# Performance work log

Measured on AMD Instinct MI355X. Metric: run time of the kernel, lower is better.

Reference implementation:

```python
import jax, jax.numpy as jnp
import numpy as np

T, H, W_, CIN, LAT, HID, OUT, NHL = 32, 64, 64, 3, 256, 256, 3, 3
OMEGA = 30.0  # SIREN sine frequency


def _uniform(key, shape, fan_in):
    b = np.sqrt(6.0 / fan_in) / OMEGA
    return jax.random.uniform(key, shape, jnp.float32, -b, b)


def setup_inputs() -> dict:
    key = jax.random.key(0)
    ks = jax.random.split(key, 10)
    return {
        "coords": jax.random.normal(ks[0], (T, H, W_, CIN), jnp.float32),
        "latents": jax.random.normal(ks[1], (T, LAT), jnp.float32),
        # shared SIREN weights (nf_net): W stored as (out, in) like nn.Linear
        "W0": _uniform(ks[2], (HID, CIN), CIN),
        "b0": jnp.zeros((HID,), jnp.float32),
        "Wh": _uniform(ks[3], (NHL, HID, HID), HID),
        "bh": jnp.zeros((NHL, HID), jnp.float32),
        "Wf": _uniform(ks[4], (OUT, HID), HID),
        "bf": jnp.zeros((OUT,), jnp.float32),
        # hypernet weight generators (hw_net), no bias
        "HW0": _uniform(ks[5], (HID * CIN, LAT), LAT),
        "HWh": _uniform(ks[6], (NHL, HID * HID, LAT), LAT),
        # hypernet bias generators (hb_net), no bias
        "HB": _uniform(ks[7], (NHL + 1, HID, LAT), LAT),
    }


def reference(coords, latents, W0, b0, Wh, bh, Wf, bf, HW0, HWh, HB):
    t = latents.shape[0]
    # per-frame hyper biases for all layers: (t, NHL+1, HID)
    hb = jnp.einsum('tl,khl->tkh', latents, HB)
    # layer 0: per-frame weight (t, HID, CIN)
    hw0 = (latents @ HW0.T).reshape(t, HID, CIN)
    x = coords  # (t,h,w,CIN)
    x = (x @ W0.T + b0
         + jnp.einsum('thwi,toi->thwo', x, hw0)
         + hb[:, 0][:, None, None, :])
    x = jnp.sin(OMEGA * x)
    for i in range(NHL):
        hw = (latents @ HWh[i].T).reshape(t, HID, HID)  # (t, HID, HID)
        x = (x @ Wh[i].T + bh[i]
             + jnp.einsum('thwi,toi->thwo', x, hw)
             + hb[:, i + 1][:, None, None, :])
        x = jnp.sin(OMEGA * x)
    return x @ Wf.T + bf  # (t,h,w,OUT)
```

## Files before the change

### kernel.cpp

```cpp
#include <hip/hip_runtime.h>
#include <cstdint>
#include <cstddef>

typedef __attribute__((ext_vector_type(8))) _Float16 f16x8;
typedef __attribute__((ext_vector_type(16))) float f32x16;

#define LO_SCALE 2048.0f
#define LO_INV   (1.0f / 2048.0f)

union H8 { f16x8 v; _Float16 h[8]; };

__global__ __launch_bounds__(256) void kab(
    const float* __restrict__ latents, const float* __restrict__ W0,
    const float* __restrict__ b0, const float* __restrict__ bh,
    const float* __restrict__ HW0, const float* __restrict__ HB,
    const float* __restrict__ Wh, const float* __restrict__ HWh,
    _Float16* __restrict__ w0blob, float* __restrict__ beff,
    _Float16* __restrict__ whblob) {
  __shared__ float lat_t[8192];
  int tid = threadIdx.x, bid = blockIdx.x;

  if (bid >= 768) {
    int id = (bid - 768) * 256 + tid;
    if (id < 32768) {
      int t = id >> 10, rem = id & 1023;
      int r2 = rem & 127, part = r2 >> 6, lane = r2 & 63;
      int nf = rem >> 7;
      int o = nf * 32 + (lane & 31), kc = lane >> 5;
      const float* lat = latents + t * 256;
      H8 outv;
#pragma unroll
      for (int j = 0; j < 8; ++j) outv.h[j] = (_Float16)0.0f;
#pragma unroll
      for (int j = 0; j < 8; ++j) {
        int i = kc * 8 + j;
        if (i < 3) {
          const float* row = HW0 + (o * 3 + i) * 256;
          float s = W0[o * 3 + i];
          for (int k = 0; k < 256; k += 4)
            s += row[k] * lat[k] + row[k + 1] * lat[k + 1] +
                 row[k + 2] * lat[k + 2] + row[k + 3] * lat[k + 3];
          _Float16 hi = (_Float16)s;
          outv.h[j] = part ? (_Float16)((s - (float)hi) * LO_SCALE) : hi;
        }
      }
      *(f16x8*)(w0blob + (size_t)id * 8) = outv.v;
    } else {
      int v = id - 32768;
      int t = v >> 10, k = (v >> 8) & 3, hm = v & 255;
      float base = (k == 0) ? b0[hm] : bh[(k - 1) * 256 + hm];
      const float* lat = latents + t * 256;
      const float* row = HB + (size_t)(k * 256 + hm) * 256;
      float s = base;
      for (int kk = 0; kk < 256; kk += 4)
        s += row[kk] * lat[kk] + row[kk + 1] * lat[kk + 1] +
             row[kk + 2] * lat[kk + 2] + row[kk + 3] * lat[kk + 3];
      beff[v] = s;
    }
    return;
  }

  int h = bid & 1, ks = (bid >> 1) & 15, nf = (bid >> 5) & 7, l = bid >> 8;

  {
    int f = tid >> 3, kb = (tid & 7) * 32;
#pragma unroll
    for (int m = 0; m < 32; m += 4) {
      float4 v = *(const float4*)(latents + f * 256 + kb + m);
      lat_t[(kb + m + 0) * 32 + f] = v.x;
      lat_t[(kb + m + 1) * 32 + f] = v.y;
      lat_t[(kb + m + 2) * 32 + f] = v.z;
      lat_t[(kb + m + 3) * 32 + f] = v.w;
    }
  }
  __syncthreads();

  int oo = tid >> 3, jj = tid & 7;
  int o = nf * 32 + oo;
  int i = ks * 16 + h * 8 + jj;
  int r = o * 256 + i;
  const float* rowp = HWh + ((size_t)l * 65536 + (size_t)r) * 256;

  float acc[32];
#pragma unroll
  for (int f = 0; f < 32; ++f) acc[f] = 0.f;

  float curf[16], nxtf[16];
#pragma unroll
  for (int q = 0; q < 4; ++q)
    *(float4*)(curf + q * 4) = *(const float4*)(rowp + q * 4);

  for (int kc = 0; kc < 16; ++kc) {
    if (kc < 15) {
#pragma unroll
      for (int q = 0; q < 4; ++q)
        *(float4*)(nxtf + q * 4) = *(const float4*)(rowp + (kc + 1) * 16 + q * 4);
    }
    const float* lp = lat_t + kc * 512;
#pragma unroll
    for (int m = 0; m < 16; ++m) {
      float hw = curf[m];
#pragma unroll
      for (int fq = 0; fq < 8; ++fq) {
        float4 lv = *(const float4*)(lp + m * 32 + fq * 4);
        acc[fq * 4 + 0] += hw * lv.x;
        acc[fq * 4 + 1] += hw * lv.y;
        acc[fq * 4 + 2] += hw * lv.z;
        acc[fq * 4 + 3] += hw * lv.w;
      }
    }
#pragma unroll
    for (int q = 0; q < 16; ++q) curf[q] = nxtf[q];
  }

  float whv = Wh[l * 65536 + r];
  size_t cbase = (size_t)(nf * 16 + ks) * 1024 + (size_t)h * 256 + (size_t)tid;
#pragma unroll
  for (int t = 0; t < 32; ++t) {
    float w = acc[t] + whv;
    _Float16 hi = (_Float16)w;
    _Float16 lo = (_Float16)((w - (float)hi) * LO_SCALE);
    size_t b = (size_t)(t * 3 + l) * 131072 + cbase;
    whblob[b] = hi;
    whblob[b + 512] = lo;
  }
}

__global__ __launch_bounds__(256, 2) void kb_siren(
    const float* __restrict__ coords, const _Float16* __restrict__ whblob,
    const _Float16* __restrict__ w0blob, const float* __restrict__ beff,
    const float* __restrict__ Wf, const float* __restrict__ bf,
    float* __restrict__ out) {
  __shared__ _Float16 xs_hi[64 * 264];
  __shared__ _Float16 xs_lo[64 * 264];
  __shared__ float wf_s[768];
  __shared__ float red[768];
  int tid = threadIdx.x;
  int bid0 = blockIdx.x;
  int bid = (bid0 & 7) * 256 + (bid0 >> 3);
  int t = bid >> 6, tile = bid & 63;
  int wv = tid >> 6, lane = tid & 63, col = lane & 31, h = lane >> 5;

  if (tid < 192) *(float4*)(wf_s + tid * 4) = *(const float4*)(Wf + tid * 4);
  if (tid < 64) {
    const float* cp = coords + (size_t)(t * 4096 + tile * 64 + tid) * 3;
    float c0 = cp[0], c1 = cp[1], c2 = cp[2];
    H8 hv, lv, z;
#pragma unroll
    for (int j = 0; j < 8; ++j) { hv.h[j] = (_Float16)0.f; lv.h[j] = (_Float16)0.f; z.h[j] = (_Float16)0.f; }
    _Float16 h0 = (_Float16)c0, h1 = (_Float16)c1, h2 = (_Float16)c2;
    hv.h[0] = h0; hv.h[1] = h1; hv.h[2] = h2;
    lv.h[0] = (_Float16)((c0 - (float)h0) * LO_SCALE);
    lv.h[1] = (_Float16)((c1 - (float)h1) * LO_SCALE);
    lv.h[2] = (_Float16)((c2 - (float)h2) * LO_SCALE);
    *(f16x8*)(xs_hi + tid * 264) = hv.v;
    *(f16x8*)(xs_lo + tid * 264) = lv.v;
    *(f16x8*)(xs_hi + tid * 264 + 8) = z.v;
    *(f16x8*)(xs_lo + tid * 264 + 8) = z.v;
  }
  __syncthreads();

  f32x16 accA[2][2], accB[2][2];

  auto init_bias = [&](int bk) {
#pragma unroll
    for (int fr = 0; fr < 2; ++fr) {
      const float* bp = beff + ((t * 4 + bk) << 8) + (wv * 2 + fr) * 32 + h * 4;
#pragma unroll
      for (int rq = 0; rq < 4; ++rq) {
        float4 bvv = *(const float4*)(bp + rq * 8);
        float ba[4];
        *(float4*)ba = bvv;
#pragma unroll
        for (int q = 0; q < 4; ++q) {
          accA[fr][0][rq * 4 + q] = ba[q];
          accA[fr][1][rq * 4 + q] = ba[q];
          accB[fr][0][rq * 4 + q] = 0.f;
          accB[fr][1][rq * 4 + q] = 0.f;
        }
      }
    }
  };

  auto aload4 = [&](const _Float16* blobL, int NS, int ks,
                    f16x8& a0h, f16x8& a0l, f16x8& a1h, f16x8& a1l) {
    const _Float16* p0 = blobL + (size_t)(((wv * 2 + 0) * NS + ks) * 2) * 512 + lane * 8;
    const _Float16* p1 = blobL + (size_t)(((wv * 2 + 1) * NS + ks) * 2) * 512 + lane * 8;
    a0h = *(const f16x8*)p0;
    a0l = *(const f16x8*)(p0 + 512);
    a1h = *(const f16x8*)p1;
    a1l = *(const f16x8*)(p1 + 512);
  };

  auto mfma_step = [&](f16x8 a0h, f16x8 a0l, f16x8 a1h, f16x8 a1l, int ks) {
#pragma unroll
    for (int pf = 0; pf < 2; ++pf) {
      int off = (pf * 32 + col) * 264 + ks * 16 + h * 8;
      f16x8 bh_ = *(const f16x8*)(xs_hi + off);
      f16x8 bl_ = *(const f16x8*)(xs_lo + off);
      accA[0][pf] = __builtin_amdgcn_mfma_f32_32x32x16_f16(a0h, bh_, accA[0][pf], 0, 0, 0);
      accB[0][pf] = __builtin_amdgcn_mfma_f32_32x32x16_f16(a0h, bl_, accB[0][pf], 0, 0, 0);
      accB[0][pf] = __builtin_amdgcn_mfma_f32_32x32x16_f16(a0l, bh_, accB[0][pf], 0, 0, 0);
      accA[1][pf] = __builtin_amdgcn_mfma_f32_32x32x16_f16(a1h, bh_, accA[1][pf], 0, 0, 0);
      accB[1][pf] = __builtin_amdgcn_mfma_f32_32x32x16_f16(a1h, bl_, accB[1][pf], 0, 0, 0);
      accB[1][pf] = __builtin_amdgcn_mfma_f32_32x32x16_f16(a1l, bh_, accB[1][pf], 0, 0, 0);
    }
  };

  auto epilogue = [&]() {
#pragma unroll
    for (int fr = 0; fr < 2; ++fr)
#pragma unroll
      for (int pf = 0; pf < 2; ++pf)
#pragma unroll
        for (int r = 0; r < 16; ++r)
          accA[fr][pf][r] = __sinf(fmaf(accB[fr][pf][r], 30.0f * LO_INV, 30.0f * accA[fr][pf][r]));
    __syncthreads();
#pragma unroll
    for (int fr = 0; fr < 2; ++fr)
#pragma unroll
      for (int pf = 0; pf < 2; ++pf)
#pragma unroll
        for (int g = 0; g < 2; ++g) {
          float seq[8];
#pragma unroll
          for (int q = 0; q < 4; ++q) {
            float oa = accA[fr][pf][8 * g + q];
            float ob = accA[fr][pf][8 * g + 4 + q];
            float send = h ? oa : ob;
            float recv = __shfl_xor(send, 32, 64);
            seq[q]     = h ? recv : oa;
            seq[4 + q] = h ? ob : recv;
          }
          H8 hv, lv;
#pragma unroll
          for (int j = 0; j < 8; ++j) {
            _Float16 hi = (_Float16)seq[j];
            hv.h[j] = hi;
            lv.h[j] = (_Float16)((seq[j] - (float)hi) * LO_SCALE);
          }
          int off = (pf * 32 + col) * 264 + wv * 64 + fr * 32 + g * 16 + h * 8;
          *(f16x8*)(xs_hi + off) = hv.v;
          *(f16x8*)(xs_lo + off) = lv.v;
        }
    __syncthreads();
  };

  const _Float16* bl0 = whblob + (size_t)(t * 3) * 131072;
  f16x8 c0h, c0l, c1h, c1l, n0h, n0l, n1h, n1l;

  init_bias(0);
  aload4(w0blob + (size_t)t * 8192, 1, 0, c0h, c0l, c1h, c1l);
  mfma_step(c0h, c0l, c1h, c1l, 0);
  aload4(bl0, 16, 0, c0h, c0l, c1h, c1l);
  epilogue();

#pragma unroll
  for (int li = 0; li < 3; ++li) {
    init_bias(li + 1);
    const _Float16* bl = whblob + (size_t)(t * 3 + li) * 131072;
    const _Float16* bln = whblob + (size_t)(t * 3 + li + 1) * 131072;
#pragma unroll
    for (int ks2 = 0; ks2 < 8; ++ks2) {
      int ksA = ks2 * 2, ksB = ks2 * 2 + 1;
      aload4(bl, 16, ksB, n0h, n0l, n1h, n1l);
      mfma_step(c0h, c0l, c1h, c1l, ksA);
      if (ksB < 15) {
        aload4(bl, 16, ksB + 1, c0h, c0l, c1h, c1l);
      } else if (li < 2) {
        aload4(bln, 16, 0, c0h, c0l, c1h, c1l);
      }
      mfma_step(n0h, n0l, n1h, n1l, ksB);
    }
    epilogue();
  }

  {
    float pc0 = 0.f, pc1 = 0.f, pc2 = 0.f;
    int px = tid & 63, kq = tid >> 6;
#pragma unroll
    for (int cc = 0; cc < 8; ++cc) {
      int k0 = kq * 64 + cc * 8;
      H8 hv, lv;
      hv.v = *(const f16x8*)(xs_hi + px * 264 + k0);
      lv.v = *(const f16x8*)(xs_lo + px * 264 + k0);
#pragma unroll
      for (int j = 0; j < 8; ++j) {
        float xv = (float)hv.h[j] + (float)lv.h[j] * LO_INV;
        pc0 += xv * wf_s[k0 + j];
        pc1 += xv * wf_s[256 + k0 + j];
        pc2 += xv * wf_s[512 + k0 + j];
      }
    }
    red[kq * 192 + px * 3 + 0] = pc0;
    red[kq * 192 + px * 3 + 1] = pc1;
    red[kq * 192 + px * 3 + 2] = pc2;
    __syncthreads();
    if (tid < 192) {
      int p2 = tid / 3, c = tid - p2 * 3;
      float s = bf[c];
#pragma unroll
      for (int q = 0; q < 4; ++q) s += red[q * 192 + p2 * 3 + c];
      out[(size_t)(t * 4096 + tile * 64 + p2) * 3 + c] = s;
    }
  }
}

extern "C" void kernel_launch(void* const* d_in, const int* in_sizes, int n_in,
                              void* d_out, int out_size, void* d_ws, size_t ws_size,
                              hipStream_t stream) {
  const float* coords  = (const float*)d_in[0];
  const float* latents = (const float*)d_in[1];
  const float* W0      = (const float*)d_in[2];
  const float* b0      = (const float*)d_in[3];
  const float* Wh      = (const float*)d_in[4];
  const float* bh      = (const float*)d_in[5];
  const float* Wf      = (const float*)d_in[6];
  const float* bf      = (const float*)d_in[7];
  const float* HW0     = (const float*)d_in[8];
  const float* HWh     = (const float*)d_in[9];
  const float* HB      = (const float*)d_in[10];
  float* outp = (float*)d_out;

  char* w = (char*)d_ws;
  _Float16* whblob = (_Float16*)w;
  _Float16* w0blob = (_Float16*)(w + 25165824);
  float*    beff   = (float*)(w + 25690112);

  kab<<<1024, 256, 0, stream>>>(latents, W0, b0, bh, HW0, HB, Wh, HWh,
                                w0blob, beff, whblob);
  kb_siren<<<2048, 256, 0, stream>>>(coords, whblob, w0blob, beff, Wf, bf, outp);
}
```

Measured before the change: 230.0 us.

## Prescale weights by omega/2pi, use fract+v_sin, drop shuffles in epilogue stores

```diff
diff --git a/kernel.cpp b/kernel.cpp
--- a/kernel.cpp
+++ b/kernel.cpp
@@ -3,12 +3,15 @@
 #include <cstddef>
 
 typedef __attribute__((ext_vector_type(8))) _Float16 f16x8;
+typedef __attribute__((ext_vector_type(2))) __fp16 h2;
 typedef __attribute__((ext_vector_type(16))) float f32x16;
 
 #define LO_SCALE 2048.0f
 #define LO_INV   (1.0f / 2048.0f)
+#define OMEGA_SC 4.774648292756860f
 
 union H8 { f16x8 v; _Float16 h[8]; };
+union U2 { h2 v[2]; uint2 u; };
 
 __global__ __launch_bounds__(256) void kab(
     const float* __restrict__ latents, const float* __restrict__ W0,
@@ -40,6 +43,7 @@
           for (int k = 0; k < 256; k += 4)
             s += row[k] * lat[k] + row[k + 1] * lat[k + 1] +
                  row[k + 2] * lat[k + 2] + row[k + 3] * lat[k + 3];
+          s *= OMEGA_SC;
           _Float16 hi = (_Float16)s;
           outv.h[j] = part ? (_Float16)((s - (float)hi) * LO_SCALE) : hi;
         }
@@ -55,7 +59,7 @@
       for (int kk = 0; kk < 256; kk += 4)
         s += row[kk] * lat[kk] + row[kk + 1] * lat[kk + 1] +
              row[kk + 2] * lat[kk + 2] + row[kk + 3] * lat[kk + 3];
-      beff[v] = s;
+      beff[v] = s * OMEGA_SC;
     }
     return;
   }
@@ -117,7 +121,7 @@
   size_t cbase = (size_t)(nf * 16 + ks) * 1024 + (size_t)h * 256 + (size_t)tid;
 #pragma unroll
   for (int t = 0; t < 32; ++t) {
-    float w = acc[t] + whv;
+    float w = (acc[t] + whv) * OMEGA_SC;
     _Float16 hi = (_Float16)w;
     _Float16 lo = (_Float16)((w - (float)hi) * LO_SCALE);
     size_t b = (size_t)(t * 3 + l) * 131072 + cbase;
@@ -148,11 +152,11 @@
     H8 hv, lv, z;
 #pragma unroll
     for (int j = 0; j < 8; ++j) { hv.h[j] = (_Float16)0.f; lv.h[j] = (_Float16)0.f; z.h[j] = (_Float16)0.f; }
-    _Float16 h0 = (_Float16)c0, h1 = (_Float16)c1, h2 = (_Float16)c2;
-    hv.h[0] = h0; hv.h[1] = h1; hv.h[2] = h2;
+    _Float16 h0 = (_Float16)c0, h1 = (_Float16)c1, h2_ = (_Float16)c2;
+    hv.h[0] = h0; hv.h[1] = h1; hv.h[2] = h2_;
     lv.h[0] = (_Float16)((c0 - (float)h0) * LO_SCALE);
     lv.h[1] = (_Float16)((c1 - (float)h1) * LO_SCALE);
-    lv.h[2] = (_Float16)((c2 - (float)h2) * LO_SCALE);
+    lv.h[2] = (_Float16)((c2 - (float)h2_) * LO_SCALE);
     *(f16x8*)(xs_hi + tid * 264) = hv.v;
     *(f16x8*)(xs_lo + tid * 264) = lv.v;
     *(f16x8*)(xs_hi + tid * 264 + 8) = z.v;
@@ -207,6 +211,13 @@
     }
   };
 
+  auto sin2pi = [](float x) {
+    float f, r;
+    asm("v_fract_f32 %0, %1" : "=v"(f) : "v"(x));
+    asm("v_sin_f32 %0, %1" : "=v"(r) : "v"(f));
+    return r;
+  };
+
   auto epilogue = [&]() {
 #pragma unroll
     for (int fr = 0; fr < 2; ++fr)
@@ -214,35 +225,35 @@
       for (int pf = 0; pf < 2; ++pf)
 #pragma unroll
         for (int r = 0; r < 16; ++r)
-          accA[fr][pf][r] = __sinf(fmaf(accB[fr][pf][r], 30.0f * LO_INV, 30.0f * accA[fr][pf][r]));
+          accA[fr][pf][r] = sin2pi(fmaf(accB[fr][pf][r], LO_INV, accA[fr][pf][r]));
     __syncthreads();
 #pragma unroll
     for (int fr = 0; fr < 2; ++fr)
 #pragma unroll
-      for (int pf = 0; pf < 2; ++pf)
-#pragma unroll
-        for (int g = 0; g < 2; ++g) {
-          float seq[8];
-#pragma unroll
-          for (int q = 0; q < 4; ++q) {
-            float oa = accA[fr][pf][8 * g + q];
-            float ob = accA[fr][pf][8 * g + 4 + q];
-            float send = h ? oa : ob;
-            float recv = __shfl_xor(send, 32, 64);
-            seq[q]     = h ? recv : oa;
-            seq[4 + q] = h ? ob : recv;
-          }
-          H8 hv, lv;
-#pragma unroll
-          for (int j = 0; j < 8; ++j) {
-            _Float16 hi = (_Float16)seq[j];
-            hv.h[j] = hi;
-            lv.h[j] = (_Float16)((seq[j] - (float)hi) * LO_SCALE);
-          }
-          int off = (pf * 32 + col) * 264 + wv * 64 + fr * 32 + g * 16 + h * 8;
-          *(f16x8*)(xs_hi + off) = hv.v;
-          *(f16x8*)(xs_lo + off) = lv.v;
+      for (int pf = 0; pf < 2; ++pf) {
+        int base = (pf * 32 + col) * 264 + wv * 64 + fr * 32 + h * 4;
+#pragma unroll
+        for (int qd = 0; qd < 4; ++qd) {
+          float v0 = accA[fr][pf][qd * 4 + 0];
+          float v1 = accA[fr][pf][qd * 4 + 1];
+          float v2 = accA[fr][pf][qd * 4 + 2];
+          float v3 = accA[fr][pf][qd * 4 + 3];
+          h2 ha = __builtin_amdgcn_cvt_pkrtz(v0, v1);
+          h2 hb = __builtin_amdgcn_cvt_pkrtz(v2, v3);
+          float l0 = (v0 - (float)ha[0]) * LO_SCALE;
+          float l1 = (v1 - (float)ha[1]) * LO_SCALE;
+          float l2 = (v2 - (float)hb[0]) * LO_SCALE;
+          float l3 = (v3 - (float)hb[1]) * LO_SCALE;
+          h2 la = __builtin_amdgcn_cvt_pkrtz(l0, l1);
+          h2 lb = __builtin_amdgcn_cvt_pkrtz(l2, l3);
+          U2 uh, ul;
+          uh.v[0] = ha; uh.v[1] = hb;
+          ul.v[0] = la; ul.v[1] = lb;
+          int off = base + qd * 8;
+          *(uint2*)(xs_hi + off) = uh.u;
+          *(uint2*)(xs_lo + off) = ul.u;
         }
+      }
     __syncthreads();
   };
 
```

Measured after the change: 216.3 us. 1.06x faster.
